# Kernel optimization log

Measured on AMD Instinct MI355X. Metric: run time of the kernel, lower is better.

Reference implementation:

```python
import jax, jax.numpy as jnp
import numpy as np

N_USERS = 50000
N_ITEMS = 150000
N = N_USERS + N_ITEMS
N_EDGES = 1250000
D = 64
N_LAYERS = 3


def setup_inputs() -> dict:
    key = jax.random.key(0)
    ks = jax.random.split(key, 7)
    edge_src = jax.random.randint(ks[0], (N_EDGES,), 0, N, dtype=jnp.int32)
    edge_dst = jax.random.randint(ks[1], (N_EDGES,), 0, N, dtype=jnp.int32)
    edge_weight = jax.random.uniform(ks[2], (N_EDGES,), dtype=jnp.float32)
    user_emb = jax.random.normal(ks[3], (N_USERS, D), dtype=jnp.float32) * 0.1
    item_emb = jax.random.normal(ks[4], (N_ITEMS, D), dtype=jnp.float32) * 0.1
    # Ws[layer, which_linear] with which_linear in {0: W1 (on L@e), 1: W2 (on (L@e)*e), 2: W3 (on e)}
    Ws = jax.random.normal(ks[5], (N_LAYERS, 3, D, D), dtype=jnp.float32) * (1.0 / np.sqrt(D))
    bs = jnp.zeros((N_LAYERS, 3, D), dtype=jnp.float32)
    return {"edge_src": edge_src, "edge_dst": edge_dst, "edge_weight": edge_weight,
            "user_emb": user_emb, "item_emb": item_emb, "Ws": Ws, "bs": bs}


def _l2_normalize(x):
    # torch.nn.functional.normalize(p=2, dim=1, eps=1e-12)
    n = jnp.sqrt(jnp.sum(x * x, axis=1, keepdims=True))
    return x / jnp.maximum(n, 1e-12)


def reference(edge_src, edge_dst, edge_weight, user_emb, item_emb, Ws, bs):
    e = jnp.concatenate([user_emb, item_emb], axis=0)  # [N, D]
    all_embs = [e]
    for i in range(N_LAYERS):
        # SpMM: term1 = L @ e (COO scatter-add)
        term1 = jax.ops.segment_sum(edge_weight[:, None] * e[edge_src], edge_dst,
                                    num_segments=N)  # [N, D]
        term2 = term1 * e
        inter = (term1 @ Ws[i, 0] + bs[i, 0]
                 + term2 @ Ws[i, 1] + bs[i, 1]
                 + e @ Ws[i, 2] + bs[i, 2])
        inter = jax.nn.leaky_relu(inter, negative_slope=0.01)
        e = _l2_normalize(inter)  # dropout is identity in eval mode
        all_embs.append(e)
    all_embs = jnp.concatenate(all_embs, axis=1)  # [N, 4*D]
    return all_embs[:N_USERS], all_embs[N_USERS:]
```

## Files before the change

kernel.cpp:

```cpp
#include <hip/hip_runtime.h>
#include <hip/hip_bf16.h>

#define NU 50000
#define NI 150000
#define NN 200000
#define NE 1250000
#define DD 64
#define NLAYERS 3
#define SCAN_B 1024
#define NB ((NN + SCAN_B - 1) / SCAN_B)
#define BT_STRIDE 232

typedef __attribute__((ext_vector_type(8))) short bf16x8;
typedef __attribute__((ext_vector_type(4))) float f32x4;

static __device__ __forceinline__ unsigned short f2b(float x) {
  __hip_bfloat16 h = __float2bfloat16(x);
  return *reinterpret_cast<unsigned short*>(&h);
}

static __device__ __forceinline__ unsigned int pack2(float lo, float hi) {
  return (unsigned int)f2b(lo) | ((unsigned int)f2b(hi) << 16);
}

static __device__ __forceinline__ bf16x8 pack8(float4 a, float4 b) {
  union { bf16x8 v; unsigned short u[8]; } r;
  r.u[0] = f2b(a.x); r.u[1] = f2b(a.y); r.u[2] = f2b(a.z); r.u[3] = f2b(a.w);
  r.u[4] = f2b(b.x); r.u[5] = f2b(b.y); r.u[6] = f2b(b.z); r.u[7] = f2b(b.w);
  return r.v;
}

static __device__ __forceinline__ float4 m4(float4 a, float4 b) {
  float4 r; r.x = a.x * b.x; r.y = a.y * b.y; r.z = a.z * b.z; r.w = a.w * b.w; return r;
}

__global__ __launch_bounds__(256) void k_init(const float4* __restrict__ ue,
                                              const float4* __restrict__ ie,
                                              float4* __restrict__ out4,
                                              uint2* __restrict__ ebf2) {
  int gid = blockIdx.x * 256 + threadIdx.x;
  if (gid >= NN * 16) return;
  int row = gid >> 4, q = gid & 15;
  float4 v = (row < NU) ? ue[(size_t)row * 16 + q] : ie[(size_t)(row - NU) * 16 + q];
  out4[(size_t)row * 64 + q] = v;
  uint2 b; b.x = pack2(v.x, v.y); b.y = pack2(v.z, v.w);
  ebf2[(size_t)row * 16 + q] = b;
}

__global__ __launch_bounds__(256) void k_hist(const int* __restrict__ dst, int* __restrict__ cnt) {
  int e = blockIdx.x * 256 + threadIdx.x;
  if (e < NE) atomicAdd(&cnt[dst[e]], 1);
}

__global__ __launch_bounds__(SCAN_B) void k_scan1(const int* __restrict__ cnt,
                                                  int* __restrict__ local,
                                                  int* __restrict__ btot) {
  __shared__ int sm[SCAN_B];
  int t = threadIdx.x;
  int i = blockIdx.x * SCAN_B + t;
  int v = (i < NN) ? cnt[i] : 0;
  sm[t] = v;
  __syncthreads();
  for (int off = 1; off < SCAN_B; off <<= 1) {
    int x = (t >= off) ? sm[t - off] : 0;
    __syncthreads();
    sm[t] += x;
    __syncthreads();
  }
  if (i < NN) local[i] = sm[t] - v;
  if (t == SCAN_B - 1) btot[blockIdx.x] = sm[t];
}

__global__ __launch_bounds__(256) void k_scan2(int* __restrict__ btot) {
  __shared__ int sm[256];
  int t = threadIdx.x;
  int v = (t < NB) ? btot[t] : 0;
  sm[t] = v;
  __syncthreads();
  for (int off = 1; off < 256; off <<= 1) {
    int x = (t >= off) ? sm[t - off] : 0;
    __syncthreads();
    sm[t] += x;
    __syncthreads();
  }
  if (t < NB) btot[t] = sm[t] - v;
}

__global__ __launch_bounds__(256) void k_finalize(const int* __restrict__ local,
                                                  const int* __restrict__ btot,
                                                  int* __restrict__ row_start,
                                                  int* __restrict__ cursor) {
  int i = blockIdx.x * 256 + threadIdx.x;
  if (i < NN) {
    int v = local[i] + btot[i / SCAN_B];
    row_start[i] = v;
    cursor[i] = v;
  }
  if (i == 0) row_start[NN] = NE;
}

__global__ __launch_bounds__(256) void k_fill(const int* __restrict__ src,
                                              const int* __restrict__ dst,
                                              const float* __restrict__ w,
                                              int* __restrict__ cursor,
                                              int2* __restrict__ csr_pack) {
  int e = blockIdx.x * 256 + threadIdx.x;
  if (e < NE) {
    int p = atomicAdd(&cursor[dst[e]], 1);
    int2 pk; pk.x = src[e]; pk.y = __float_as_int(w[e]);
    csr_pack[p] = pk;
  }
}

__global__ __launch_bounds__(256) void k_spmm(const int* __restrict__ row_start,
                                              const int2* __restrict__ csr_pack,
                                              const unsigned int* __restrict__ ebf,
                                              float* __restrict__ term1) {
  int gid = blockIdx.x * 256 + threadIdx.x;
  int row = gid >> 6;
  if (row >= NN) return;
  int l = gid & 63;
  int h = l >> 5;
  int c = l & 31;
  int s0 = row_start[row];
  int s1 = row_start[row + 1];
  float a0 = 0.f, a1 = 0.f;
  for (int base = s0; base < s1; base += 8) {
    int j0 = base + 0 + h, j1 = base + 2 + h, j2 = base + 4 + h, j3 = base + 6 + h;
    int2 p0 = csr_pack[j0 < s1 ? j0 : s0];
    int2 p1 = csr_pack[j1 < s1 ? j1 : s0];
    int2 p2 = csr_pack[j2 < s1 ? j2 : s0];
    int2 p3 = csr_pack[j3 < s1 ? j3 : s0];
    unsigned int v0 = ebf[(size_t)p0.x * 32 + c];
    unsigned int v1 = ebf[(size_t)p1.x * 32 + c];
    unsigned int v2 = ebf[(size_t)p2.x * 32 + c];
    unsigned int v3 = ebf[(size_t)p3.x * 32 + c];
    float w0 = (j0 < s1) ? __int_as_float(p0.y) : 0.f;
    float w1 = (j1 < s1) ? __int_as_float(p1.y) : 0.f;
    float w2 = (j2 < s1) ? __int_as_float(p2.y) : 0.f;
    float w3 = (j3 < s1) ? __int_as_float(p3.y) : 0.f;
    a0 = fmaf(w0, __uint_as_float(v0 << 16), a0);
    a1 = fmaf(w0, __uint_as_float(v0 & 0xffff0000u), a1);
    a0 = fmaf(w1, __uint_as_float(v1 << 16), a0);
    a1 = fmaf(w1, __uint_as_float(v1 & 0xffff0000u), a1);
    a0 = fmaf(w2, __uint_as_float(v2 << 16), a0);
    a1 = fmaf(w2, __uint_as_float(v2 & 0xffff0000u), a1);
    a0 = fmaf(w3, __uint_as_float(v3 << 16), a0);
    a1 = fmaf(w3, __uint_as_float(v3 & 0xffff0000u), a1);
  }
  a0 += __shfl_xor(a0, 32, 64);
  a1 += __shfl_xor(a1, 32, 64);
  if (h == 0) {
    float2 st; st.x = a0; st.y = a1;
    reinterpret_cast<float2*>(term1 + (size_t)row * 64)[c] = st;
  }
}

__global__ __launch_bounds__(256) void k_row_mfma(const float* __restrict__ term1,
                                                  const float* __restrict__ Ws,
                                                  const float* __restrict__ bs,
                                                  float* __restrict__ out,
                                                  unsigned short* __restrict__ ebf_next,
                                                  int layer) {
  __shared__ unsigned short Bt[64][BT_STRIDE];
  const int tid = threadIdx.x;
  const float* __restrict__ Wl = Ws + (size_t)layer * 3 * 4096;
  {
    int n = tid & 63;
    int jb = (tid >> 6) * 48;
#pragma unroll 4
    for (int j = jb; j < jb + 48; ++j) {
      Bt[n][j] = f2b(Wl[(size_t)j * 64 + n]);
    }
  }
  __syncthreads();

  const int l = tid & 63;
  const int wv = tid >> 6;
  const int g = l >> 4;
  const int li = l & 15;
  const int rowbase = blockIdx.x * 64 + wv * 16;
  const int r = rowbase + li;

  const float4* __restrict__ t1p = reinterpret_cast<const float4*>(term1 + (size_t)r * 64);
  const float4* __restrict__ ep  = reinterpret_cast<const float4*>(out + (size_t)r * 256 + (size_t)layer * 64);
  float4 ta0 = t1p[2 * g], ta1 = t1p[2 * g + 1];
  float4 tb0 = t1p[8 + 2 * g], tb1 = t1p[8 + 2 * g + 1];
  float4 ea0 = ep[2 * g], ea1 = ep[2 * g + 1];
  float4 eb0 = ep[8 + 2 * g], eb1 = ep[8 + 2 * g + 1];

  bf16x8 Afr[6];
  Afr[0] = pack8(ta0, ta1);
  Afr[1] = pack8(tb0, tb1);
  Afr[2] = pack8(m4(ta0, ea0), m4(ta1, ea1));
  Afr[3] = pack8(m4(tb0, eb0), m4(tb1, eb1));
  Afr[4] = pack8(ea0, ea1);
  Afr[5] = pack8(eb0, eb1);

  const float* __restrict__ bsl = bs + (size_t)layer * 3 * 64;
  f32x4 acc[4];
#pragma unroll
  for (int f = 0; f < 4; ++f) {
    int n = f * 16 + li;
    float bv = bsl[n] + bsl[64 + n] + bsl[128 + n];
    acc[f] = (f32x4){bv, bv, bv, bv};
  }

#pragma unroll
  for (int s = 0; s < 6; ++s) {
#pragma unroll
    for (int f = 0; f < 4; ++f) {
      const bf16x8 Bf = *reinterpret_cast<const bf16x8*>(&Bt[f * 16 + li][s * 32 + 8 * g]);
      acc[f] = __builtin_amdgcn_mfma_f32_16x16x32_bf16(Afr[s], Bf, acc[f], 0, 0, 0);
    }
  }

  float p[4];
#pragma unroll
  for (int reg = 0; reg < 4; ++reg) {
    float ssum = 0.f;
#pragma unroll
    for (int f = 0; f < 4; ++f) {
      float x = acc[f][reg];
      x = (x >= 0.f) ? x : 0.01f * x;
      acc[f][reg] = x;
      ssum = fmaf(x, x, ssum);
    }
    p[reg] = ssum;
  }
#pragma unroll
  for (int off = 1; off < 16; off <<= 1) {
#pragma unroll
    for (int reg = 0; reg < 4; ++reg) p[reg] += __shfl_xor(p[reg], off, 64);
  }
  float inv[4];
#pragma unroll
  for (int reg = 0; reg < 4; ++reg) inv[reg] = 1.0f / fmaxf(sqrtf(p[reg]), 1e-12f);

  float* __restrict__ ob = out + (size_t)(layer + 1) * 64;
  const bool wbf = (layer + 1) < NLAYERS;
#pragma unroll
  for (int reg = 0; reg < 4; ++reg) {
#pragma unroll
    for (int f = 0; f < 4; ++f) {
      float val = acc[f][reg] * inv[reg];
      ob[(size_t)(rowbase + 4 * g + reg) * 256 + f * 16 + li] = val;
      if (wbf) ebf_next[(size_t)(rowbase + 4 * g + reg) * 64 + f * 16 + li] = f2b(val);
    }
  }
}

extern "C" void kernel_launch(void* const* d_in, const int* in_sizes, int n_in,
                              void* d_out, int out_size, void* d_ws, size_t ws_size,
                              hipStream_t stream) {
  const int* edge_src = (const int*)d_in[0];
  const int* edge_dst = (const int*)d_in[1];
  const float* edge_w = (const float*)d_in[2];
  const float* user_emb = (const float*)d_in[3];
  const float* item_emb = (const float*)d_in[4];
  const float* Ws = (const float*)d_in[5];
  const float* bs = (const float*)d_in[6];
  float* out = (float*)d_out;

  char* w = (char*)d_ws;
  float* term1 = (float*)w;       w += (size_t)NN * 64 * 4;
  unsigned int* ebf = (unsigned int*)w; w += (size_t)NN * 32 * 4;
  int2* csr_pack = (int2*)w;      w += (size_t)NE * 8;
  int* cnt = (int*)w;             w += (size_t)NN * 4;
  int* local = (int*)w;           w += (size_t)NN * 4;
  int* row_start = (int*)w;       w += (size_t)(NN + 4) * 4;
  int* cursor = (int*)w;          w += (size_t)NN * 4;
  int* btot = (int*)w;            w += 256 * 4;

  hipMemsetAsync(cnt, 0, (size_t)NN * 4, stream);
  k_init<<<(NN * 16 + 255) / 256, 256, 0, stream>>>(
      (const float4*)user_emb, (const float4*)item_emb, (float4*)out, (uint2*)ebf);
  k_hist<<<(NE + 255) / 256, 256, 0, stream>>>(edge_dst, cnt);
  k_scan1<<<NB, SCAN_B, 0, stream>>>(cnt, local, btot);
  k_scan2<<<1, 256, 0, stream>>>(btot);
  k_finalize<<<(NN + 255) / 256, 256, 0, stream>>>(local, btot, row_start, cursor);
  k_fill<<<(NE + 255) / 256, 256, 0, stream>>>(edge_src, edge_dst, edge_w, cursor, csr_pack);

  for (int layer = 0; layer < NLAYERS; ++layer) {
    k_spmm<<<(NN * 64 + 255) / 256, 256, 0, stream>>>(row_start, csr_pack, ebf, term1);
    k_row_mfma<<<NN / 64, 256, 0, stream>>>(term1, Ws, bs, out, (unsigned short*)ebf, layer);
  }
}
```

Before: 454.7 us.

## Fuse SpMM gather into per-layer MFMA kernel with LDS term1 and ping-pong bf16 buffers

Merges the SpMM and dense-transform kernels into a single per-layer kernel. Each wave gathers neighbour embeddings for its 16 rows one row at a time, prefetching the next row's CSR entries, and writes term1 as bf16 into LDS, so the fp32 term1 round trip through global memory goes away. It reads e from the bf16 buffer instead of the fp32 output and double-buffers ebf to avoid read/write hazards. In exchange, each wave now handles 16 rows serially, which cuts gather parallelism, and term1*e is computed in bf16, which loses some precision.

Result: faster. 416.1 us (-8.5%).

```diff
diff --git a/kernel.cpp b/kernel.cpp
--- a/kernel.cpp
+++ b/kernel.cpp
@@ -10,6 +10,7 @@
 #define SCAN_B 1024
 #define NB ((NN + SCAN_B - 1) / SCAN_B)
 #define BT_STRIDE 232
+#define T1_STRIDE 72
 
 typedef __attribute__((ext_vector_type(8))) short bf16x8;
 typedef __attribute__((ext_vector_type(4))) float f32x4;
@@ -23,15 +24,22 @@
   return (unsigned int)f2b(lo) | ((unsigned int)f2b(hi) << 16);
 }
 
-static __device__ __forceinline__ bf16x8 pack8(float4 a, float4 b) {
-  union { bf16x8 v; unsigned short u[8]; } r;
-  r.u[0] = f2b(a.x); r.u[1] = f2b(a.y); r.u[2] = f2b(a.z); r.u[3] = f2b(a.w);
-  r.u[4] = f2b(b.x); r.u[5] = f2b(b.y); r.u[6] = f2b(b.z); r.u[7] = f2b(b.w);
-  return r.v;
-}
-
-static __device__ __forceinline__ float4 m4(float4 a, float4 b) {
-  float4 r; r.x = a.x * b.x; r.y = a.y * b.y; r.z = a.z * b.z; r.w = a.w * b.w; return r;
+static __device__ __forceinline__ float blo(unsigned int u) { return __uint_as_float(u << 16); }
+static __device__ __forceinline__ float bhi(unsigned int u) { return __uint_as_float(u & 0xffff0000u); }
+
+static __device__ __forceinline__ bf16x8 mulbf8(bf16x8 a, bf16x8 b) {
+  union { bf16x8 v; unsigned int u[4]; } A, B, R;
+  A.v = a; B.v = b;
+#pragma unroll
+  for (int i = 0; i < 4; ++i) {
+    R.u[i] = pack2(blo(A.u[i]) * blo(B.u[i]), bhi(A.u[i]) * bhi(B.u[i]));
+  }
+  return R.v;
+}
+
+__global__ __launch_bounds__(256) void k_zero(int* __restrict__ p) {
+  int i = blockIdx.x * 256 + threadIdx.x;
+  if (i < NN) p[i] = 0;
 }
 
 __global__ __launch_bounds__(256) void k_init(const float4* __restrict__ ue,
@@ -112,90 +120,114 @@
   }
 }
 
-__global__ __launch_bounds__(256) void k_spmm(const int* __restrict__ row_start,
-                                              const int2* __restrict__ csr_pack,
-                                              const unsigned int* __restrict__ ebf,
-                                              float* __restrict__ term1) {
-  int gid = blockIdx.x * 256 + threadIdx.x;
-  int row = gid >> 6;
-  if (row >= NN) return;
-  int l = gid & 63;
-  int h = l >> 5;
-  int c = l & 31;
-  int s0 = row_start[row];
-  int s1 = row_start[row + 1];
-  float a0 = 0.f, a1 = 0.f;
-  for (int base = s0; base < s1; base += 8) {
-    int j0 = base + 0 + h, j1 = base + 2 + h, j2 = base + 4 + h, j3 = base + 6 + h;
-    int2 p0 = csr_pack[j0 < s1 ? j0 : s0];
-    int2 p1 = csr_pack[j1 < s1 ? j1 : s0];
-    int2 p2 = csr_pack[j2 < s1 ? j2 : s0];
-    int2 p3 = csr_pack[j3 < s1 ? j3 : s0];
-    unsigned int v0 = ebf[(size_t)p0.x * 32 + c];
-    unsigned int v1 = ebf[(size_t)p1.x * 32 + c];
-    unsigned int v2 = ebf[(size_t)p2.x * 32 + c];
-    unsigned int v3 = ebf[(size_t)p3.x * 32 + c];
-    float w0 = (j0 < s1) ? __int_as_float(p0.y) : 0.f;
-    float w1 = (j1 < s1) ? __int_as_float(p1.y) : 0.f;
-    float w2 = (j2 < s1) ? __int_as_float(p2.y) : 0.f;
-    float w3 = (j3 < s1) ? __int_as_float(p3.y) : 0.f;
-    a0 = fmaf(w0, __uint_as_float(v0 << 16), a0);
-    a1 = fmaf(w0, __uint_as_float(v0 & 0xffff0000u), a1);
-    a0 = fmaf(w1, __uint_as_float(v1 << 16), a0);
-    a1 = fmaf(w1, __uint_as_float(v1 & 0xffff0000u), a1);
-    a0 = fmaf(w2, __uint_as_float(v2 << 16), a0);
-    a1 = fmaf(w2, __uint_as_float(v2 & 0xffff0000u), a1);
-    a0 = fmaf(w3, __uint_as_float(v3 << 16), a0);
-    a1 = fmaf(w3, __uint_as_float(v3 & 0xffff0000u), a1);
-  }
-  a0 += __shfl_xor(a0, 32, 64);
-  a1 += __shfl_xor(a1, 32, 64);
-  if (h == 0) {
-    float2 st; st.x = a0; st.y = a1;
-    reinterpret_cast<float2*>(term1 + (size_t)row * 64)[c] = st;
-  }
-}
-
-__global__ __launch_bounds__(256) void k_row_mfma(const float* __restrict__ term1,
-                                                  const float* __restrict__ Ws,
-                                                  const float* __restrict__ bs,
-                                                  float* __restrict__ out,
-                                                  unsigned short* __restrict__ ebf_next,
-                                                  int layer) {
+__global__ __launch_bounds__(256) void k_layer(const int* __restrict__ row_start,
+                                               const int2* __restrict__ csr_pack,
+                                               const unsigned int* __restrict__ ebf,
+                                               const float* __restrict__ Ws,
+                                               const float* __restrict__ bs,
+                                               float* __restrict__ out,
+                                               unsigned short* __restrict__ ebf_next,
+                                               int layer, int wbf) {
   __shared__ unsigned short Bt[64][BT_STRIDE];
+  __shared__ unsigned short t1s[4][16][T1_STRIDE];
+
   const int tid = threadIdx.x;
   const float* __restrict__ Wl = Ws + (size_t)layer * 3 * 4096;
   {
     int n = tid & 63;
     int jb = (tid >> 6) * 48;
 #pragma unroll 4
-    for (int j = jb; j < jb + 48; ++j) {
-      Bt[n][j] = f2b(Wl[(size_t)j * 64 + n]);
-    }
+    for (int j = jb; j < jb + 48; ++j) Bt[n][j] = f2b(Wl[(size_t)j * 64 + n]);
   }
   __syncthreads();
 
   const int l = tid & 63;
   const int wv = tid >> 6;
+  const int rbase = blockIdx.x * 64 + wv * 16;
+
+  {
+    const int h = l >> 5, c = l & 31;
+    int rs = row_start[rbase + (l < 16 ? l : 16)];
+
+    int2 q0, q1, q2, q3;
+    {
+      int b = __shfl(rs, 0, 64), e = __shfl(rs, 1, 64);
+      int j;
+      j = b + 0 + h; q0 = csr_pack[j < e ? j : 0];
+      j = b + 2 + h; q1 = csr_pack[j < e ? j : 0];
+      j = b + 4 + h; q2 = csr_pack[j < e ? j : 0];
+      j = b + 6 + h; q3 = csr_pack[j < e ? j : 0];
+    }
+#pragma unroll 1
+    for (int rr = 0; rr < 16; ++rr) {
+      int s0 = __shfl(rs, rr, 64), s1 = __shfl(rs, rr + 1, 64);
+      float a0 = 0.f, a1 = 0.f;
+      unsigned int v0 = 0, v1 = 0, v2 = 0, v3 = 0;
+      float w0 = 0.f, w1 = 0.f, w2 = 0.f, w3 = 0.f;
+      const bool any = s0 < s1;
+      if (any) {
+        v0 = ebf[(size_t)q0.x * 32 + c];
+        v1 = ebf[(size_t)q1.x * 32 + c];
+        v2 = ebf[(size_t)q2.x * 32 + c];
+        v3 = ebf[(size_t)q3.x * 32 + c];
+        w0 = (s0 + 0 + h < s1) ? __int_as_float(q0.y) : 0.f;
+        w1 = (s0 + 2 + h < s1) ? __int_as_float(q1.y) : 0.f;
+        w2 = (s0 + 4 + h < s1) ? __int_as_float(q2.y) : 0.f;
+        w3 = (s0 + 6 + h < s1) ? __int_as_float(q3.y) : 0.f;
+      }
+      int2 n0, n1, n2, n3;
+      {
+        int b = __shfl(rs, rr + 1, 64), e = __shfl(rs, rr + 2 <= 16 ? rr + 2 : 16, 64);
+        int j;
+        j = b + 0 + h; n0 = csr_pack[j < e ? j : 0];
+        j = b + 2 + h; n1 = csr_pack[j < e ? j : 0];
+        j = b + 4 + h; n2 = csr_pack[j < e ? j : 0];
+        j = b + 6 + h; n3 = csr_pack[j < e ? j : 0];
+      }
+      if (any) {
+        a0 = fmaf(w0, blo(v0), a0); a1 = fmaf(w0, bhi(v0), a1);
+        a0 = fmaf(w1, blo(v1), a0); a1 = fmaf(w1, bhi(v1), a1);
+        a0 = fmaf(w2, blo(v2), a0); a1 = fmaf(w2, bhi(v2), a1);
+        a0 = fmaf(w3, blo(v3), a0); a1 = fmaf(w3, bhi(v3), a1);
+        for (int base = s0 + 8; base < s1; base += 8) {
+          int2 t0, t1_, t2, t3;
+          int j;
+          j = base + 0 + h; t0 = csr_pack[j < s1 ? j : 0];
+          j = base + 2 + h; t1_ = csr_pack[j < s1 ? j : 0];
+          j = base + 4 + h; t2 = csr_pack[j < s1 ? j : 0];
+          j = base + 6 + h; t3 = csr_pack[j < s1 ? j : 0];
+          unsigned int u0 = ebf[(size_t)t0.x * 32 + c];
+          unsigned int u1 = ebf[(size_t)t1_.x * 32 + c];
+          unsigned int u2 = ebf[(size_t)t2.x * 32 + c];
+          unsigned int u3 = ebf[(size_t)t3.x * 32 + c];
+          float x0 = (base + 0 + h < s1) ? __int_as_float(t0.y) : 0.f;
+          float x1 = (base + 2 + h < s1) ? __int_as_float(t1_.y) : 0.f;
+          float x2 = (base + 4 + h < s1) ? __int_as_float(t2.y) : 0.f;
+          float x3 = (base + 6 + h < s1) ? __int_as_float(t3.y) : 0.f;
+          a0 = fmaf(x0, blo(u0), a0); a1 = fmaf(x0, bhi(u0), a1);
+          a0 = fmaf(x1, blo(u1), a0); a1 = fmaf(x1, bhi(u1), a1);
+          a0 = fmaf(x2, blo(u2), a0); a1 = fmaf(x2, bhi(u2), a1);
+          a0 = fmaf(x3, blo(u3), a0); a1 = fmaf(x3, bhi(u3), a1);
+        }
+      }
+      a0 += __shfl_xor(a0, 32, 64);
+      a1 += __shfl_xor(a1, 32, 64);
+      if (h == 0) *reinterpret_cast<unsigned int*>(&t1s[wv][rr][2 * c]) = pack2(a0, a1);
+      q0 = n0; q1 = n1; q2 = n2; q3 = n3;
+    }
+  }
+
   const int g = l >> 4;
   const int li = l & 15;
-  const int rowbase = blockIdx.x * 64 + wv * 16;
-  const int r = rowbase + li;
-
-  const float4* __restrict__ t1p = reinterpret_cast<const float4*>(term1 + (size_t)r * 64);
-  const float4* __restrict__ ep  = reinterpret_cast<const float4*>(out + (size_t)r * 256 + (size_t)layer * 64);
-  float4 ta0 = t1p[2 * g], ta1 = t1p[2 * g + 1];
-  float4 tb0 = t1p[8 + 2 * g], tb1 = t1p[8 + 2 * g + 1];
-  float4 ea0 = ep[2 * g], ea1 = ep[2 * g + 1];
-  float4 eb0 = ep[8 + 2 * g], eb1 = ep[8 + 2 * g + 1];
-
-  bf16x8 Afr[6];
-  Afr[0] = pack8(ta0, ta1);
-  Afr[1] = pack8(tb0, tb1);
-  Afr[2] = pack8(m4(ta0, ea0), m4(ta1, ea1));
-  Afr[3] = pack8(m4(tb0, eb0), m4(tb1, eb1));
-  Afr[4] = pack8(ea0, ea1);
-  Afr[5] = pack8(eb0, eb1);
+  const int r = rbase + li;
+
+  bf16x8 A0 = *reinterpret_cast<const bf16x8*>(&t1s[wv][li][8 * g]);
+  bf16x8 A1 = *reinterpret_cast<const bf16x8*>(&t1s[wv][li][32 + 8 * g]);
+  const unsigned short* __restrict__ eb = reinterpret_cast<const unsigned short*>(ebf);
+  bf16x8 E0 = *reinterpret_cast<const bf16x8*>(eb + (size_t)r * 64 + 8 * g);
+  bf16x8 E1 = *reinterpret_cast<const bf16x8*>(eb + (size_t)r * 64 + 32 + 8 * g);
+  bf16x8 T0 = mulbf8(A0, E0);
+  bf16x8 T1 = mulbf8(A1, E1);
 
   const float* __restrict__ bsl = bs + (size_t)layer * 3 * 64;
   f32x4 acc[4];
@@ -206,6 +238,7 @@
     acc[f] = (f32x4){bv, bv, bv, bv};
   }
 
+  bf16x8 Afr[6] = {A0, A1, T0, T1, E0, E1};
 #pragma unroll
   for (int s = 0; s < 6; ++s) {
 #pragma unroll
@@ -238,14 +271,13 @@
   for (int reg = 0; reg < 4; ++reg) inv[reg] = 1.0f / fmaxf(sqrtf(p[reg]), 1e-12f);
 
   float* __restrict__ ob = out + (size_t)(layer + 1) * 64;
-  const bool wbf = (layer + 1) < NLAYERS;
 #pragma unroll
   for (int reg = 0; reg < 4; ++reg) {
 #pragma unroll
     for (int f = 0; f < 4; ++f) {
       float val = acc[f][reg] * inv[reg];
-      ob[(size_t)(rowbase + 4 * g + reg) * 256 + f * 16 + li] = val;
-      if (wbf) ebf_next[(size_t)(rowbase + 4 * g + reg) * 64 + f * 16 + li] = f2b(val);
+      ob[(size_t)(rbase + 4 * g + reg) * 256 + f * 16 + li] = val;
+      if (wbf) ebf_next[(size_t)(rbase + 4 * g + reg) * 64 + f * 16 + li] = f2b(val);
     }
   }
 }
@@ -263,8 +295,8 @@
   float* out = (float*)d_out;
 
   char* w = (char*)d_ws;
-  float* term1 = (float*)w;       w += (size_t)NN * 64 * 4;
-  unsigned int* ebf = (unsigned int*)w; w += (size_t)NN * 32 * 4;
+  unsigned int* ebfA = (unsigned int*)w; w += (size_t)NN * 32 * 4;
+  unsigned int* ebfB = (unsigned int*)w; w += (size_t)NN * 32 * 4;
   int2* csr_pack = (int2*)w;      w += (size_t)NE * 8;
   int* cnt = (int*)w;             w += (size_t)NN * 4;
   int* local = (int*)w;           w += (size_t)NN * 4;
@@ -272,17 +304,19 @@
   int* cursor = (int*)w;          w += (size_t)NN * 4;
   int* btot = (int*)w;            w += 256 * 4;
 
-  hipMemsetAsync(cnt, 0, (size_t)NN * 4, stream);
+  k_zero<<<(NN + 255) / 256, 256, 0, stream>>>(cnt);
   k_init<<<(NN * 16 + 255) / 256, 256, 0, stream>>>(
-      (const float4*)user_emb, (const float4*)item_emb, (float4*)out, (uint2*)ebf);
+      (const float4*)user_emb, (const float4*)item_emb, (float4*)out, (uint2*)ebfA);
   k_hist<<<(NE + 255) / 256, 256, 0, stream>>>(edge_dst, cnt);
   k_scan1<<<NB, SCAN_B, 0, stream>>>(cnt, local, btot);
   k_scan2<<<1, 256, 0, stream>>>(btot);
   k_finalize<<<(NN + 255) / 256, 256, 0, stream>>>(local, btot, row_start, cursor);
   k_fill<<<(NE + 255) / 256, 256, 0, stream>>>(edge_src, edge_dst, edge_w, cursor, csr_pack);
 
-  for (int layer = 0; layer < NLAYERS; ++layer) {
-    k_spmm<<<(NN * 64 + 255) / 256, 256, 0, stream>>>(row_start, csr_pack, ebf, term1);
-    k_row_mfma<<<NN / 64, 256, 0, stream>>>(term1, Ws, bs, out, (unsigned short*)ebf, layer);
-  }
-}
+  k_layer<<<NN / 64, 256, 0, stream>>>(row_start, csr_pack, ebfA, Ws, bs, out,
+                                       (unsigned short*)ebfB, 0, 1);
+  k_layer<<<NN / 64, 256, 0, stream>>>(row_start, csr_pack, ebfB, Ws, bs, out,
+                                       (unsigned short*)ebfA, 1, 1);
+  k_layer<<<NN / 64, 256, 0, stream>>>(row_start, csr_pack, ebfA, Ws, bs, out,
+                                       (unsigned short*)ebfB, 2, 0);
+}
```
